# Performance work log

Hardware: AMD Instinct MI355X
Metric: run time of the kernel (lower is better)

The kernel has to match this reference:

```python
import jax, jax.numpy as jnp
import numpy as np
import math

D_MODEL = 256
N_HEAD = 1
C_IN = 32
B, L = 8, 2048
FACTOR = 5


def _pos_encoding(L, D):
    pos = jnp.arange(L, dtype=jnp.float32)[:, None]
    div = jnp.exp(jnp.arange(0, D, 2, dtype=jnp.float32) * (-math.log(10000.0) / D))
    pe = jnp.zeros((L, D), dtype=jnp.float32)
    pe = pe.at[:, 0::2].set(jnp.sin(pos * div))
    pe = pe.at[:, 1::2].set(jnp.cos(pos * div))
    return pe


def _layer_norm(x, g, b, eps=1e-5):
    mu = x.mean(-1, keepdims=True)
    var = ((x - mu) ** 2).mean(-1, keepdims=True)
    return (x - mu) / jnp.sqrt(var + eps) * g + b


def setup_inputs():
    key = jax.random.key(0)
    ks = jax.random.split(key, 16)
    D = D_MODEL
    s = 0.02
    p = {}
    p["x"] = jax.random.normal(ks[0], (B, L, C_IN), jnp.float32)
    sample_k = min(FACTOR * math.ceil(math.log(L)), L)  # = 40 for L=2048
    p["sample_idx"] = jax.random.randint(ks[1], (L, sample_k), 0, L)
    p["emb_w"] = jax.random.normal(ks[2], (C_IN, N_HEAD * D)) * s
    p["emb_b"] = jnp.zeros((N_HEAD * D,))
    for i, n in enumerate(["wq", "wk", "wv", "wo"]):
        p[n] = jax.random.normal(ks[3 + i], (D, D)) * s
        p["b" + n[1]] = jnp.zeros((D,))
    p["conv1_w"] = jax.random.normal(ks[7], (D, D)) * s  # Conv1d kernel=1 == linear, d_ff = d_model
    p["conv1_b"] = jnp.zeros((D,))
    p["conv2_w"] = jax.random.normal(ks[8], (D, D)) * s
    p["conv2_b"] = jnp.zeros((D,))
    for n in ["ln1", "ln2", "lnf"]:
        p[n + "_g"] = jnp.ones((D,))
        p[n + "_b"] = jnp.zeros((D,))
    p["gru_wih"] = jax.random.normal(ks[9], (3 * D, D)) * s
    p["gru_whh"] = jax.random.normal(ks[10], (3 * D, D)) * s
    p["gru_bih"] = jnp.zeros((3 * D,))
    p["gru_bhh"] = jnp.zeros((3 * D,))
    p["fc_w"] = jax.random.normal(ks[11], (D, 1)) * s
    p["fc_b"] = jnp.zeros((1,))
    return p


def _forward(x, sample_idx, emb_w, emb_b, wq, bq, wk, bk, wv, bv, wo, bo,
             conv1_w, conv1_b, conv2_w, conv2_b, ln1_g, ln1_b, ln2_g, ln2_b,
             lnf_g, lnf_b, gru_wih, gru_whh, gru_bih, gru_bhh, fc_w, fc_b):
    Bx, Lx, _ = x.shape
    H = N_HEAD
    src = x @ emb_w + emb_b + _pos_encoding(Lx, emb_w.shape[1])  # [B,L,D]
    D = src.shape[-1]
    dk = D // H

    def heads(t, w, b):
        return (t @ w + b).reshape(Bx, Lx, H, dk).transpose(0, 2, 1, 3)  # [B,H,L,dk]

    Q = heads(src, wq, bq)
    K = heads(src, wk, bk)
    V = heads(src, wv, bv)

    # ---- ProbSparse attention (Informer, non-masked) ----
    u = sample_idx.shape[1]                                  # n_top == sample_k here
    K_sample = K[:, :, sample_idx, :]                        # [B,H,L,s,dk]
    QK_s = jnp.einsum("bhld,bhlsd->bhls", Q, K_sample)
    M = QK_s.max(-1) - QK_s.sum(-1) / Lx                     # sparsity measure per query
    _, top = jax.lax.top_k(M, u)                             # [B,H,u]
    Q_red = jnp.take_along_axis(Q, top[..., None], axis=2)   # [B,H,u,dk]
    scores = jnp.einsum("bhud,bhkd->bhuk", Q_red, K) / jnp.sqrt(jnp.float32(dk))
    attn = jax.nn.softmax(scores, axis=-1)
    upd = jnp.einsum("bhuk,bhkd->bhud", attn, V)             # [B,H,u,dk]
    ctx = jnp.broadcast_to(V.mean(axis=2, keepdims=True), Q.shape)  # initial context = mean(V)
    bi = jnp.arange(Bx)[:, None, None]
    hi = jnp.arange(H)[None, :, None]
    ctx = ctx.at[bi, hi, top].set(upd)
    out = ctx.transpose(0, 2, 1, 3).reshape(Bx, Lx, D) @ wo + bo

    # ---- EncoderLayer FFN (Conv1d k=1 -> gelu -> Conv1d k=1), residuals, norms ----
    x1 = _layer_norm(src + out, ln1_g, ln1_b)
    y = jax.nn.gelu(x1 @ conv1_w + conv1_b, approximate=False)
    y = y @ conv2_w + conv2_b
    enc = _layer_norm(_layer_norm(x1 + y, ln2_g, ln2_b), lnf_g, lnf_b)

    # ---- GRU: faithful to source bug: seq-major nn.GRU fed [B,L,D] -> scans over batch dim ----
    def step(h, xt):
        gi = xt @ gru_wih.T + gru_bih
        gh = h @ gru_whh.T + gru_bhh
        ir, iz, inn = jnp.split(gi, 3, axis=-1)
        hr, hz, hn = jnp.split(gh, 3, axis=-1)
        r = jax.nn.sigmoid(ir + hr)
        z = jax.nn.sigmoid(iz + hz)
        n = jnp.tanh(inn + r * hn)
        h = (1.0 - z) * n + z * h
        return h, h

    h0 = jnp.zeros((Lx, enc.shape[-1]), enc.dtype)
    _, gru_out = jax.lax.scan(step, h0, enc)  # [B,L,D]
    return gru_out[:, -1, :] @ fc_w + fc_b    # [B,1]


def reference(x, sample_idx, emb_w, emb_b, wq, bq, wk, bk, wv, bv, wo, bo,
              conv1_w, conv1_b, conv2_w, conv2_b, ln1_g, ln1_b, ln2_g, ln2_b,
              lnf_g, lnf_b, gru_wih, gru_whh, gru_bih, gru_bhh, fc_w, fc_b):
    return _forward(x, sample_idx, emb_w, emb_b, wq, bq, wk, bk, wv, bv, wo, bo,
                    conv1_w, conv1_b, conv2_w, conv2_b, ln1_g, ln1_b, ln2_g, ln2_b,
                    lnf_g, lnf_b, gru_wih, gru_whh, gru_bih, gru_bhh, fc_w, fc_b)
```

## Files before the change

### kernel.cpp

```cpp
#include <hip/hip_runtime.h>
#include <hip/hip_bf16.h>
#include <math.h>

#define BB 8
#define LL 2048
#define CIN 32
#define DD 256
#define UU 40
#define NROW (BB*LL)
#define NSL  (NROW*DD)
#define GB 8

typedef unsigned short u16;
typedef __attribute__((ext_vector_type(8))) short short8;
typedef __attribute__((ext_vector_type(4))) float f32x4;

__device__ __forceinline__ u16 f2bf(float v) {
    unsigned u = __float_as_uint(v);
    unsigned r = (u + 0x7FFF + ((u >> 16) & 1)) >> 16;
    return (u16)r;
}
__device__ __forceinline__ float bf2f(u16 h) {
    return __uint_as_float(((unsigned)h) << 16);
}

template<int CTRL>
__device__ __forceinline__ float dpp_add(float v) {
    int s = __builtin_amdgcn_update_dpp(0, __float_as_int(v), CTRL, 0xf, 0xf, true);
    return v + __int_as_float(s);
}
__device__ __forceinline__ float row16_sum(float v) {
    v = dpp_add<0x118>(v);
    v = dpp_add<0x114>(v);
    v = dpp_add<0x112>(v);
    v = dpp_add<0x111>(v);
    return v;
}
__device__ __forceinline__ float dot4(float4 a, float4 b) {
    return a.x * b.x + a.y * b.y + a.z * b.z + a.w * b.w;
}
__device__ __forceinline__ float4 nt_load4(const float* p) {
    f32x4 v = __builtin_nontemporal_load((const f32x4*)p);
    float4 r; r.x = v.x; r.y = v.y; r.z = v.z; r.w = v.w;
    return r;
}

__global__ __launch_bounds__(256) void src_kernel(
    const float* __restrict__ x, const float* __restrict__ emb_w,
    const float* __restrict__ emb_b,
    u16* __restrict__ srch, u16* __restrict__ srcl, float* __restrict__ srcrow)
{
    __shared__ float xs[CIN];
    const int orig = blockIdx.x;
    const int b = orig & 7;
    const int l = orig >> 3;
    const int r = (b << 11) | l;
    const int d = threadIdx.x;
    if (d < CIN) xs[d] = x[(size_t)r * CIN + d];
    __syncthreads();
    float acc = emb_b[d];
#pragma unroll 8
    for (int c = 0; c < CIN; ++c) acc += xs[c] * emb_w[c * DD + d];
    const int i = d >> 1;
    const float ang = (float)l * expf((float)(2 * i) * (-9.210340371976184f / 256.0f));
    const float pe = (d & 1) ? cosf(ang) : sinf(ang);
    const float v = acc + pe;
    const u16 h = f2bf(v);
    srch[(size_t)r * DD + d] = h;
    srcl[(size_t)r * DD + d] = f2bf(v - bf2f(h));
    if (l == LL - 1) srcrow[b * DD + d] = v;
}

__global__ __launch_bounds__(256) void splitw_kernel(
    const float* __restrict__ wq, const float* __restrict__ wk,
    const float* __restrict__ wv, u16* __restrict__ whT, u16* __restrict__ wlT)
{
    const int o = blockIdx.x, n = blockIdx.y, k = threadIdx.x;
    const float* W = (o == 0) ? wq : (o == 1) ? wk : wv;
    const float v = W[(size_t)k * DD + n];
    const u16 h = f2bf(v);
    whT[((size_t)o << 16) + n * DD + k] = h;
    wlT[((size_t)o << 16) + n * DD + k] = f2bf(v - bf2f(h));
}

__global__ __launch_bounds__(256) void gemm_qkv_mfma(
    const u16* __restrict__ srch, const u16* __restrict__ srcl,
    const u16* __restrict__ whT, const u16* __restrict__ wlT,
    const float* __restrict__ bq, const float* __restrict__ bk,
    const float* __restrict__ bv,
    float* __restrict__ Qf, float* __restrict__ K, float* __restrict__ V,
    float* __restrict__ qrow)
{
    __shared__ __align__(16) u16 AhS[64][40], AlS[64][40], BhS[64][40], BlS[64][40];
    const int t = threadIdx.x;
    const int bx = blockIdx.x;
    const int mt = (bx & 7) * 32 + (bx >> 3);
    const int bm = mt * 64;
    const int bn = blockIdx.y * 64;
    const int o  = blockIdx.z;
    const u16* wh = whT + ((size_t)o << 16);
    const u16* wl = wlT + ((size_t)o << 16);
    const float* bias = (o == 0) ? bq : (o == 1) ? bk : bv;
    float* C = (o == 0) ? Qf : (o == 1) ? K : V;

    const int srow = t >> 2, sk8 = (t & 3) * 8;
    const int lane = t & 63, w = t >> 6;
    const int frow = lane & 15, kg = (lane >> 4) * 8;

    f32x4 acc[4];
#pragma unroll
    for (int nf = 0; nf < 4; ++nf) acc[nf] = (f32x4){0.f, 0.f, 0.f, 0.f};

    for (int ks = 0; ks < 8; ++ks) {
        const int kb = ks * 32 + sk8;
        *(short8*)&AhS[srow][sk8] = *(const short8*)&srch[(size_t)(bm + srow) * DD + kb];
        *(short8*)&AlS[srow][sk8] = *(const short8*)&srcl[(size_t)(bm + srow) * DD + kb];
        *(short8*)&BhS[srow][sk8] = *(const short8*)&wh[(size_t)(bn + srow) * DD + kb];
        *(short8*)&BlS[srow][sk8] = *(const short8*)&wl[(size_t)(bn + srow) * DD + kb];
        __syncthreads();
        const short8 ah = *(const short8*)&AhS[w * 16 + frow][kg];
        const short8 al = *(const short8*)&AlS[w * 16 + frow][kg];
#pragma unroll
        for (int nf = 0; nf < 4; ++nf) {
            const short8 bh = *(const short8*)&BhS[nf * 16 + frow][kg];
            const short8 bl = *(const short8*)&BlS[nf * 16 + frow][kg];
            acc[nf] = __builtin_amdgcn_mfma_f32_16x16x32_bf16(al, bh, acc[nf], 0, 0, 0);
            acc[nf] = __builtin_amdgcn_mfma_f32_16x16x32_bf16(ah, bl, acc[nf], 0, 0, 0);
            acc[nf] = __builtin_amdgcn_mfma_f32_16x16x32_bf16(ah, bh, acc[nf], 0, 0, 0);
        }
        __syncthreads();
    }
#pragma unroll
    for (int nf = 0; nf < 4; ++nf) {
#pragma unroll
        for (int r = 0; r < 4; ++r) {
            const int row = bm + w * 16 + (lane >> 4) * 4 + r;
            const int col = bn + nf * 16 + (lane & 15);
            const float v = acc[nf][r] + bias[col];
            C[(size_t)row * DD + col] = v;
            if (o == 0 && (row & (LL - 1)) == (LL - 1))
                qrow[(row >> 11) * DD + col] = v;
        }
    }
}

__global__ __launch_bounds__(256, 4) void qks_probe(
    const float* __restrict__ Qf, const float* __restrict__ Kf,
    const int* __restrict__ sidx, float* __restrict__ M)
{
    __shared__ float qk[4][UU];
    const int bid = blockIdx.x;
    const int b = bid & 7;
    const int grp = bid >> 3;
    const int t = threadIdx.x;
    const int wv = t >> 6;
    const int lane = t & 63;
    const int sub = lane >> 4;
    const int j = lane & 15;
    const int l = grp * 4 + wv;
    const size_t r = ((size_t)b << 11) + l;

    const int* si = sidx + (size_t)l * UU;
    const int myidx = __builtin_nontemporal_load(si + (lane < UU ? lane : 0));

    const float* q = &Qf[r * DD];
    const float4 q0 = nt_load4(q + j * 16 + 0);
    const float4 q1 = nt_load4(q + j * 16 + 4);
    const float4 q2 = nt_load4(q + j * 16 + 8);
    const float4 q3 = nt_load4(q + j * 16 + 12);
    const float* Kb = Kf + ((size_t)b << 11) * DD;

    int idxs[UU / 4];
#pragma unroll
    for (int i = 0; i < UU / 4; ++i) idxs[i] = __shfl(myidx, i * 4 + sub);

    float4 kv[5][4];
#pragma unroll
    for (int i = 0; i < 5; ++i) {
        const float4* kr = (const float4*)&Kb[(size_t)idxs[i] * DD] + j * 4;
        kv[i][0] = kr[0]; kv[i][1] = kr[1]; kv[i][2] = kr[2]; kv[i][3] = kr[3];
    }

#pragma unroll
    for (int i = 0; i < UU / 4; ++i) {
        const int s = i % 5;
        float d = dot4(q0, kv[s][0]) + dot4(q1, kv[s][1])
                + dot4(q2, kv[s][2]) + dot4(q3, kv[s][3]);
        if (i + 5 < UU / 4) {
            const float4* kr = (const float4*)&Kb[(size_t)idxs[i + 5] * DD] + j * 4;
            kv[s][0] = kr[0]; kv[s][1] = kr[1]; kv[s][2] = kr[2]; kv[s][3] = kr[3];
        }
        d = row16_sum(d);
        if (j == 15) qk[wv][i * 4 + sub] = d;
    }
    __syncthreads();
    if (t < 4) {
        float mx = -1e30f, sm = 0.0f;
#pragma unroll
        for (int s = 0; s < UU; ++s) { float v = qk[t][s]; mx = fmaxf(mx, v); sm += v; }
        M[((size_t)b << 11) + grp * 4 + t] = mx - sm * (1.0f / (float)LL);
    }
}

__global__ __launch_bounds__(256) void rank_kernel(
    const float* __restrict__ M, int* __restrict__ flag)
{
    __shared__ int redi[256];
    const int b = blockIdx.x, t = threadIdx.x;
    const float* Mb = M + (size_t)b * LL;
    const float ref = Mb[LL - 1];
    int cnt = 0;
    for (int l = t; l < LL; l += 256)
        if (l != LL - 1 && Mb[l] >= ref) cnt++;
    redi[t] = cnt; __syncthreads();
    for (int s = 128; s; s >>= 1) { if (t < s) redi[t] += redi[t + s]; __syncthreads(); }
    if (t == 0) flag[b] = (redi[0] < UU) ? 1 : 0;
}

__global__ __launch_bounds__(256) void ctx_scores(
    const float* __restrict__ qrow, const float* __restrict__ K,
    const int* __restrict__ flag, float* __restrict__ sc)
{
    const int b = blockIdx.x;
    if (!flag[b]) return;
    const int t = threadIdx.x, grp = t >> 4, j = t & 15;
    const size_t base = (size_t)b * LL * DD;
    const float4* qr = (const float4*)&qrow[b * DD];
    const float4 q0 = qr[j * 4 + 0], q1 = qr[j * 4 + 1],
                 q2 = qr[j * 4 + 2], q3 = qr[j * 4 + 3];
    const int k0 = blockIdx.y * 128 + grp * 8;
#pragma unroll
    for (int i = 0; i < 8; ++i) {
        const int k = k0 + i;
        const float4* kr = (const float4*)&K[base + (size_t)k * DD];
        float d = dot4(q0, kr[j * 4 + 0]) + dot4(q1, kr[j * 4 + 1])
                + dot4(q2, kr[j * 4 + 2]) + dot4(q3, kr[j * 4 + 3]);
        d = row16_sum(d);
        if (j == 15) sc[b * LL + k] = d * (1.0f / 16.0f);
    }
}

__global__ __launch_bounds__(256) void ctx_softmax(
    const int* __restrict__ flag, float* __restrict__ sc, float* __restrict__ ssum)
{
    __shared__ float red[256];
    const int b = blockIdx.x;
    if (!flag[b]) return;
    const int t = threadIdx.x;
    float* s = sc + b * LL;
    float lm = -1e30f;
    for (int k = t; k < LL; k += 256) lm = fmaxf(lm, s[k]);
    red[t] = lm; __syncthreads();
    for (int st = 128; st; st >>= 1) { if (t < st) red[t] = fmaxf(red[t], red[t + st]); __syncthreads(); }
    const float mx = red[0]; __syncthreads();
    float ls = 0.0f;
    for (int k = t; k < LL; k += 256) { float e = expf(s[k] - mx); s[k] = e; ls += e; }
    red[t] = ls; __syncthreads();
    for (int st = 128; st; st >>= 1) { if (t < st) red[t] += red[t + st]; __syncthreads(); }
    if (t == 0) ssum[b] = red[0];
}

__global__ __launch_bounds__(256) void ctx_pv(
    const float* __restrict__ V, const float* __restrict__ sc,
    const int* __restrict__ flag, float* __restrict__ part)
{
    const int b = blockIdx.x, slice = blockIdx.y;
    const int d = threadIdx.x;
    const size_t base = (size_t)b * LL * DD;
    const int k0 = slice * 256;
    float acc = 0.0f;
    if (flag[b]) {
#pragma unroll 4
        for (int k = k0; k < k0 + 256; ++k)
            acc += sc[b * LL + k] * V[base + (size_t)k * DD + d];
    } else {
#pragma unroll 4
        for (int k = k0; k < k0 + 256; ++k)
            acc += V[base + (size_t)k * DD + d];
    }
    part[(b * 8 + slice) * DD + d] = acc;
}

__device__ __forceinline__ float block_sum256(float v, float* red) {
    const int t = threadIdx.x;
    __syncthreads();
    red[t] = v; __syncthreads();
    for (int s = 128; s; s >>= 1) { if (t < s) red[t] += red[t + s]; __syncthreads(); }
    return red[0];
}

__global__ __launch_bounds__(256) void tail_kernel(
    const float* __restrict__ srcrow, const float* __restrict__ part,
    const float* __restrict__ ssum, const int* __restrict__ flag,
    const float* __restrict__ wo, const float* __restrict__ bo,
    const float* __restrict__ c1w, const float* __restrict__ c1b,
    const float* __restrict__ c2w, const float* __restrict__ c2b,
    const float* __restrict__ g1, const float* __restrict__ b1,
    const float* __restrict__ g2, const float* __restrict__ b2,
    const float* __restrict__ gf, const float* __restrict__ bf,
    float* __restrict__ enc)
{
    __shared__ float xs[DD];
    __shared__ float red[DD];
    const int b = blockIdx.x, d = threadIdx.x;

    float cv = 0.0f;
#pragma unroll
    for (int i = 0; i < 8; ++i) cv += part[(b * 8 + i) * DD + d];
    cv = flag[b] ? cv / ssum[b] : cv * (1.0f / (float)LL);

    xs[d] = cv; __syncthreads();
    float o = bo[d];
    for (int j = 0; j < DD; ++j) o += xs[j] * wo[j * DD + d];
    const float v = srcrow[b * DD + d] + o;

    float mu = block_sum256(v, red) * (1.0f / DD);
    float dv = v - mu;
    float var = block_sum256(dv * dv, red) * (1.0f / DD);
    const float x1 = dv * rsqrtf(var + 1e-5f) * g1[d] + b1[d];

    __syncthreads(); xs[d] = x1; __syncthreads();
    float a = c1b[d];
    for (int j = 0; j < DD; ++j) a += xs[j] * c1w[j * DD + d];
    a = 0.5f * a * (1.0f + erff(a * 0.70710678118654752f));

    __syncthreads(); xs[d] = a; __syncthreads();
    float y = c2b[d];
    for (int j = 0; j < DD; ++j) y += xs[j] * c2w[j * DD + d];

    float t2 = x1 + y;
    mu = block_sum256(t2, red) * (1.0f / DD);
    dv = t2 - mu;
    var = block_sum256(dv * dv, red) * (1.0f / DD);
    float t3 = dv * rsqrtf(var + 1e-5f) * g2[d] + b2[d];

    mu = block_sum256(t3, red) * (1.0f / DD);
    dv = t3 - mu;
    var = block_sum256(dv * dv, red) * (1.0f / DD);
    enc[b * DD + d] = dv * rsqrtf(var + 1e-5f) * gf[d] + bf[d];
}

__global__ __launch_bounds__(768) void gru_coop_kernel(
    const float* __restrict__ enc, const float* __restrict__ wih,
    const float* __restrict__ whh, const float* __restrict__ bih,
    const float* __restrict__ bhh, const float* __restrict__ fcw,
    const float* __restrict__ fcb,
    unsigned long long* __restrict__ hpub,
    float* __restrict__ out)
{
    __shared__ float whhS[96][257];
    __shared__ float encS[BB][260];
    __shared__ float giS[96][8];
    __shared__ float hS[DD];
    __shared__ float ghS[96];
    __shared__ float red[256];
    const int g = blockIdx.x, t = threadIdx.x;

#pragma unroll
    for (int i = 0; i < 8; ++i) {
        const int f4 = t + 768 * i;
        const int lr = f4 >> 6, c4 = f4 & 63;
        const int R = (lr >> 5) * 256 + g * 32 + (lr & 31);
        const float4 w = *(const float4*)&whh[(size_t)R * DD + c4 * 4];
        whhS[lr][c4 * 4 + 0] = w.x; whhS[lr][c4 * 4 + 1] = w.y;
        whhS[lr][c4 * 4 + 2] = w.z; whhS[lr][c4 * 4 + 3] = w.w;
    }
    for (int e = t; e < BB * DD; e += 768) encS[e >> 8][e & 255] = enc[e];
    if (t < DD) hS[t] = 0.0f;
    __syncthreads();

    {
        const int lr = t >> 3, b = t & 7;
        const int R = (lr >> 5) * 256 + g * 32 + (lr & 31);
        float acc = bih[R];
        const float4* w4 = (const float4*)&wih[(size_t)R * DD];
#pragma unroll 8
        for (int jc = 0; jc < 64; ++jc) {
            const float4 w = w4[jc];
            acc += encS[b][jc * 4 + 0] * w.x + encS[b][jc * 4 + 1] * w.y
                 + encS[b][jc * 4 + 2] * w.z + encS[b][jc * 4 + 3] * w.w;
        }
        giS[lr][b] = acc;
    }
    __syncthreads();

    for (int step = 1; step <= BB; ++step) {
        const int b = step - 1;
        const int lr = t >> 3, s = t & 7;
        float p = 0.0f;
#pragma unroll
        for (int k = 0; k < 32; ++k) {
            const int c = s * 32 + ((k + s * 4) & 31);
            p += whhS[lr][c] * hS[c];
        }
        p = dpp_add<0x114>(p); p = dpp_add<0x112>(p); p = dpp_add<0x111>(p);
        if (s == 7) ghS[lr] = p + bhh[(lr >> 5) * 256 + g * 32 + (lr & 31)];
        __syncthreads();

        if (t < 32) {
            const float r  = 1.0f / (1.0f + expf(-(giS[t][b]      + ghS[t])));
            const float z  = 1.0f / (1.0f + expf(-(giS[32 + t][b] + ghS[32 + t])));
            const float n  = tanhf(giS[64 + t][b] + r * ghS[64 + t]);
            const float hnew = (1.0f - z) * n + z * hS[g * 32 + t];
            const unsigned long long w =
                ((unsigned long long)(unsigned)step << 32) | (unsigned long long)__float_as_uint(hnew);
            __hip_atomic_store(&hpub[g * 32 + t], w, __ATOMIC_RELAXED, __HIP_MEMORY_SCOPE_AGENT);
        }
        __syncthreads();
        if (t < DD) {
            unsigned long long w;
            do {
                w = __hip_atomic_load(&hpub[t], __ATOMIC_RELAXED, __HIP_MEMORY_SCOPE_AGENT);
            } while ((int)(w >> 32) != step);
            hS[t] = __uint_as_float((unsigned)w);
        }
        __syncthreads();

        if (g == 0) {
            if (t < DD) red[t] = hS[t] * fcw[t];
            __syncthreads();
            for (int st2 = 128; st2; st2 >>= 1) { if (t < st2) red[t] += red[t + st2]; __syncthreads(); }
            if (t == 0) out[b] = red[0] + fcb[0];
            __syncthreads();
        }
    }
}

extern "C" void kernel_launch(void* const* d_in, const int* in_sizes, int n_in,
                              void* d_out, int out_size, void* d_ws, size_t ws_size,
                              hipStream_t stream)
{
    const float* x      = (const float*)d_in[0];
    const int*   sidx   = (const int*)  d_in[1];
    const float* emb_w  = (const float*)d_in[2];
    const float* emb_b  = (const float*)d_in[3];
    const float* wq     = (const float*)d_in[4];
    const float* bq     = (const float*)d_in[5];
    const float* wk     = (const float*)d_in[6];
    const float* bk     = (const float*)d_in[7];
    const float* wv     = (const float*)d_in[8];
    const float* bv     = (const float*)d_in[9];
    const float* wo     = (const float*)d_in[10];
    const float* bo     = (const float*)d_in[11];
    const float* c1w    = (const float*)d_in[12];
    const float* c1b    = (const float*)d_in[13];
    const float* c2w    = (const float*)d_in[14];
    const float* c2b    = (const float*)d_in[15];
    const float* ln1g   = (const float*)d_in[16];
    const float* ln1b   = (const float*)d_in[17];
    const float* ln2g   = (const float*)d_in[18];
    const float* ln2b   = (const float*)d_in[19];
    const float* lnfg   = (const float*)d_in[20];
    const float* lnfb   = (const float*)d_in[21];
    const float* wih    = (const float*)d_in[22];
    const float* whh    = (const float*)d_in[23];
    const float* bih    = (const float*)d_in[24];
    const float* bhh    = (const float*)d_in[25];
    const float* fcw    = (const float*)d_in[26];
    const float* fcb    = (const float*)d_in[27];

    float* ws  = (float*)d_ws;
    float* K    = ws;
    float* V    = K + NSL;
    float* Mv   = V + NSL;
    int*   flag = (int*)(Mv + NROW);
    float* sc   = (float*)(flag + 16);
    float* ssum = sc + BB * LL;
    float* part = ssum + 16;
    float* srcrow = part + BB * 8 * DD;
    float* qrow = srcrow + BB * DD;
    float* enc  = qrow + BB * DD;
    unsigned long long* hpub = (unsigned long long*)(enc + BB * DD);
    u16* srch = (u16*)(hpub + 256);
    u16* srcl = srch + NSL;
    u16* whT  = srcl + NSL;
    u16* wlT  = whT + 3 * 65536;
    float* Qf = (float*)(wlT + 3 * 65536);

    hipMemsetAsync(hpub, 0, 256 * sizeof(unsigned long long), stream);

    splitw_kernel<<<dim3(3, 256), 256, 0, stream>>>(wq, wk, wv, whT, wlT);
    src_kernel<<<NROW, 256, 0, stream>>>(x, emb_w, emb_b, srch, srcl, srcrow);
    gemm_qkv_mfma<<<dim3(256, 4, 3), 256, 0, stream>>>(srch, srcl, whT, wlT,
                                                       bq, bk, bv, Qf, K, V, qrow);
    qks_probe<<<NROW / 4, 256, 0, stream>>>(Qf, K, sidx, Mv);
    rank_kernel<<<BB, 256, 0, stream>>>(Mv, flag);
    ctx_scores<<<dim3(BB, 16), 256, 0, stream>>>(qrow, K, flag, sc);
    ctx_softmax<<<BB, 256, 0, stream>>>(flag, sc, ssum);
    ctx_pv<<<dim3(BB, 8), 256, 0, stream>>>(V, sc, flag, part);
    tail_kernel<<<BB, 256, 0, stream>>>(srcrow, part, ssum, flag, wo, bo,
                                        c1w, c1b, c2w, c2b,
                                        ln1g, ln1b, ln2g, ln2b, lnfg, lnfb, enc);
    gru_coop_kernel<<<GB, 768, 0, stream>>>(enc, wih, whh, bih, bhh, fcw, fcb,
                                            hpub, (float*)d_out);
}
```

Measured before the change: 195.7 us.

## Stage sampled K rows into LDS via async global_load_lds in probe kernel

The Q·K sample probe now runs one 64-thread block per query row instead of four wavefronts per block. All 40 sampled K rows are issued up front as direct global-to-LDS loads. Computation is staggered with explicit vmcnt waits, so each group of four rows is consumed as it arrives, which raises memory-level parallelism compared with the register-held five-deep prefetch. In exchange it uses 40 KB of LDS per single-wave block, which limits how many blocks fit per CU, and it quadruples the block count.

```diff
diff --git a/kernel.cpp b/kernel.cpp
--- a/kernel.cpp
+++ b/kernel.cpp
@@ -43,6 +43,15 @@
     f32x4 v = __builtin_nontemporal_load((const f32x4*)p);
     float4 r; r.x = v.x; r.y = v.y; r.z = v.z; r.w = v.w;
     return r;
+}
+__device__ __forceinline__ void gload_lds16(const float* g, float* l) {
+    __builtin_amdgcn_global_load_lds(
+        (const __attribute__((address_space(1))) float*)g,
+        (__attribute__((address_space(3))) float*)l, 16, 0, 0);
+}
+template<int N> __device__ __forceinline__ void wait_vmcnt() {
+    asm volatile("s_waitcnt vmcnt(%0)" :: "n"(N) : "memory");
+    __builtin_amdgcn_sched_barrier(0);
 }
 
 __global__ __launch_bounds__(256) void src_kernel(
@@ -144,61 +153,64 @@
     }
 }
 
-__global__ __launch_bounds__(256, 4) void qks_probe(
+__global__ __launch_bounds__(64) void qks_probe(
     const float* __restrict__ Qf, const float* __restrict__ Kf,
     const int* __restrict__ sidx, float* __restrict__ M)
 {
-    __shared__ float qk[4][UU];
+    __shared__ __align__(16) float Ks[UU][256];
+    __shared__ float qk[UU];
     const int bid = blockIdx.x;
     const int b = bid & 7;
-    const int grp = bid >> 3;
+    const int l = bid >> 3;
     const int t = threadIdx.x;
-    const int wv = t >> 6;
-    const int lane = t & 63;
-    const int sub = lane >> 4;
-    const int j = lane & 15;
-    const int l = grp * 4 + wv;
-    const size_t r = ((size_t)b << 11) + l;
+    const int sub = t >> 4, j = t & 15;
 
     const int* si = sidx + (size_t)l * UU;
-    const int myidx = __builtin_nontemporal_load(si + (lane < UU ? lane : 0));
-
-    const float* q = &Qf[r * DD];
+    const int myidx = si[t < UU ? t : 0];
+
+    const float* q = &Qf[(((size_t)b << 11) + l) * DD];
     const float4 q0 = nt_load4(q + j * 16 + 0);
     const float4 q1 = nt_load4(q + j * 16 + 4);
     const float4 q2 = nt_load4(q + j * 16 + 8);
     const float4 q3 = nt_load4(q + j * 16 + 12);
+
     const float* Kb = Kf + ((size_t)b << 11) * DD;
-
-    int idxs[UU / 4];
-#pragma unroll
-    for (int i = 0; i < UU / 4; ++i) idxs[i] = __shfl(myidx, i * 4 + sub);
-
-    float4 kv[5][4];
-#pragma unroll
-    for (int i = 0; i < 5; ++i) {
-        const float4* kr = (const float4*)&Kb[(size_t)idxs[i] * DD] + j * 4;
-        kv[i][0] = kr[0]; kv[i][1] = kr[1]; kv[i][2] = kr[2]; kv[i][3] = kr[3];
-    }
-
-#pragma unroll
-    for (int i = 0; i < UU / 4; ++i) {
-        const int s = i % 5;
-        float d = dot4(q0, kv[s][0]) + dot4(q1, kv[s][1])
-                + dot4(q2, kv[s][2]) + dot4(q3, kv[s][3]);
-        if (i + 5 < UU / 4) {
-            const float4* kr = (const float4*)&Kb[(size_t)idxs[i + 5] * DD] + j * 4;
-            kv[s][0] = kr[0]; kv[s][1] = kr[1]; kv[s][2] = kr[2]; kv[s][3] = kr[3];
-        }
+    const int coff = 16 * j + 4 * sub;
+
+#pragma unroll
+    for (int s = 0; s < UU; ++s) {
+        const int idx = __builtin_amdgcn_readlane(myidx, s);
+        gload_lds16(Kb + (size_t)idx * DD + coff, &Ks[s][0]);
+    }
+
+    auto cg = [&](int i) {
+        const int sm = i * 4 + sub;
+        const float4 kv0 = *(const float4*)&Ks[sm][0 * 64 + j * 4];
+        const float4 kv1 = *(const float4*)&Ks[sm][1 * 64 + j * 4];
+        const float4 kv2 = *(const float4*)&Ks[sm][2 * 64 + j * 4];
+        const float4 kv3 = *(const float4*)&Ks[sm][3 * 64 + j * 4];
+        float d = dot4(q0, kv0) + dot4(q1, kv1)
+                + dot4(q2, kv2) + dot4(q3, kv3);
         d = row16_sum(d);
-        if (j == 15) qk[wv][i * 4 + sub] = d;
-    }
+        if (j == 15) qk[sm] = d;
+    };
+    wait_vmcnt<36>(); cg(0);
+    wait_vmcnt<32>(); cg(1);
+    wait_vmcnt<28>(); cg(2);
+    wait_vmcnt<24>(); cg(3);
+    wait_vmcnt<20>(); cg(4);
+    wait_vmcnt<16>(); cg(5);
+    wait_vmcnt<12>(); cg(6);
+    wait_vmcnt<8>();  cg(7);
+    wait_vmcnt<4>();  cg(8);
+    wait_vmcnt<0>();  cg(9);
+
     __syncthreads();
-    if (t < 4) {
+    if (t == 0) {
         float mx = -1e30f, sm = 0.0f;
 #pragma unroll
-        for (int s = 0; s < UU; ++s) { float v = qk[t][s]; mx = fmaxf(mx, v); sm += v; }
-        M[((size_t)b << 11) + grp * 4 + t] = mx - sm * (1.0f / (float)LL);
+        for (int s = 0; s < UU; ++s) { float v = qk[s]; mx = fmaxf(mx, v); sm += v; }
+        M[((size_t)b << 11) + l] = mx - sm * (1.0f / (float)LL);
     }
 }
 
@@ -483,7 +495,7 @@
     src_kernel<<<NROW, 256, 0, stream>>>(x, emb_w, emb_b, srch, srcl, srcrow);
     gemm_qkv_mfma<<<dim3(256, 4, 3), 256, 0, stream>>>(srch, srcl, whT, wlT,
                                                        bq, bk, bv, Qf, K, V, qrow);
-    qks_probe<<<NROW / 4, 256, 0, stream>>>(Qf, K, sidx, Mv);
+    qks_probe<<<NROW, 64, 0, stream>>>(Qf, K, sidx, Mv);
     rank_kernel<<<BB, 256, 0, stream>>>(Mv, flag);
     ctx_scores<<<dim3(BB, 16), 256, 0, stream>>>(qrow, K, flag, sc);
     ctx_softmax<<<BB, 256, 0, stream>>>(flag, sc, ssum);
```

Result: slower. 216.1 us (+10.4%).

## Compute sparsity probe with bf16 keys plus error bounds and exact recheck

Applied to the files above, without the earlier changes.

The QK sampling probe now reads a bf16 copy of K, which the QKV GEMM writes out, and computes an error bound for each row from absolute-value dot products. A classify pass counts rows that are certainly at or above the last row's exact measure and collects uncertain rows, which a recheck kernel then recomputes in fp32. This halves the gather bandwidth of the probe, at the cost of extra bf16 K writes, two more launches and atomics. Correctness depends on the 0.0025 error bound covering bf16 rounding of K and on the uncertain list fitting within the cap.

```diff
diff --git a/kernel.cpp b/kernel.cpp
--- a/kernel.cpp
+++ b/kernel.cpp
@@ -10,6 +10,7 @@
 #define NROW (BB*LL)
 #define NSL  (NROW*DD)
 #define GB 8
+#define UNCAP 1024
 
 typedef unsigned short u16;
 typedef __attribute__((ext_vector_type(8))) short short8;
@@ -43,6 +44,29 @@
     f32x4 v = __builtin_nontemporal_load((const f32x4*)p);
     float4 r; r.x = v.x; r.y = v.y; r.z = v.z; r.w = v.w;
     return r;
+}
+
+__device__ __forceinline__ void exact_row_qk(
+    const float* __restrict__ q, const float* __restrict__ Kb,
+    const int* __restrict__ si, int lane, int sub, int j,
+    float* qkrow)
+{
+    const int myidx = si[lane < UU ? lane : 0];
+    const float4 q0 = nt_load4(q + j * 16 + 0);
+    const float4 q1 = nt_load4(q + j * 16 + 4);
+    const float4 q2 = nt_load4(q + j * 16 + 8);
+    const float4 q3 = nt_load4(q + j * 16 + 12);
+    int idxs[UU / 4];
+#pragma unroll
+    for (int i = 0; i < UU / 4; ++i) idxs[i] = __shfl(myidx, i * 4 + sub);
+#pragma unroll
+    for (int i = 0; i < UU / 4; ++i) {
+        const float4* kr = (const float4*)&Kb[(size_t)idxs[i] * DD];
+        float d = dot4(q0, kr[j * 4 + 0]) + dot4(q1, kr[j * 4 + 1])
+                + dot4(q2, kr[j * 4 + 2]) + dot4(q3, kr[j * 4 + 3]);
+        d = row16_sum(d);
+        if (j == 15) qkrow[i * 4 + sub] = d;
+    }
 }
 
 __global__ __launch_bounds__(256) void src_kernel(
@@ -89,7 +113,7 @@
     const float* __restrict__ bq, const float* __restrict__ bk,
     const float* __restrict__ bv,
     float* __restrict__ Qf, float* __restrict__ K, float* __restrict__ V,
-    float* __restrict__ qrow)
+    float* __restrict__ qrow, u16* __restrict__ Khb)
 {
     __shared__ __align__(16) u16 AhS[64][40], AlS[64][40], BhS[64][40], BlS[64][40];
     const int t = threadIdx.x;
@@ -140,89 +164,154 @@
             C[(size_t)row * DD + col] = v;
             if (o == 0 && (row & (LL - 1)) == (LL - 1))
                 qrow[(row >> 11) * DD + col] = v;
-        }
-    }
-}
-
-__global__ __launch_bounds__(256, 4) void qks_probe(
-    const float* __restrict__ Qf, const float* __restrict__ Kf,
-    const int* __restrict__ sidx, float* __restrict__ M)
+            if (o == 1)
+                Khb[(size_t)row * DD + col] = f2bf(v);
+        }
+    }
+}
+
+__global__ __launch_bounds__(256) void qks_pass1(
+    const float* __restrict__ Qf, const u16* __restrict__ Khb,
+    const float* __restrict__ Kf, const int* __restrict__ sidx,
+    float* __restrict__ Mt, float* __restrict__ Eb,
+    float* __restrict__ M2047ex)
 {
     __shared__ float qk[4][UU];
+    __shared__ float qas[4][UU];
+    const int t = threadIdx.x;
+    const int wv = t >> 6, lane = t & 63, sub = lane >> 4, j = lane & 15;
     const int bid = blockIdx.x;
+
+    if (bid >= NROW / 4) {
+        const int b = (bid - NROW / 4) * 4 + wv;
+        const int l = LL - 1;
+        exact_row_qk(&Qf[(((size_t)b << 11) + l) * DD],
+                     Kf + ((size_t)b << 11) * DD,
+                     sidx + (size_t)l * UU, lane, sub, j, qk[wv]);
+        __syncthreads();
+        if (t < 4) {
+            const int bb = (bid - NROW / 4) * 4 + t;
+            float mx = -1e30f, sm = 0.0f;
+#pragma unroll
+            for (int s = 0; s < UU; ++s) { float v = qk[t][s]; mx = fmaxf(mx, v); sm += v; }
+            M2047ex[bb] = mx - sm * (1.0f / (float)LL);
+        }
+        return;
+    }
+
     const int b = bid & 7;
     const int grp = bid >> 3;
-    const int t = threadIdx.x;
-    const int wv = t >> 6;
-    const int lane = t & 63;
-    const int sub = lane >> 4;
-    const int j = lane & 15;
     const int l = grp * 4 + wv;
     const size_t r = ((size_t)b << 11) + l;
-
     const int* si = sidx + (size_t)l * UU;
     const int myidx = __builtin_nontemporal_load(si + (lane < UU ? lane : 0));
 
     const float* q = &Qf[r * DD];
-    const float4 q0 = nt_load4(q + j * 16 + 0);
-    const float4 q1 = nt_load4(q + j * 16 + 4);
-    const float4 q2 = nt_load4(q + j * 16 + 8);
-    const float4 q3 = nt_load4(q + j * 16 + 12);
-    const float* Kb = Kf + ((size_t)b << 11) * DD;
+    const float4 qa0 = nt_load4(q + j * 8);
+    const float4 qa1 = nt_load4(q + j * 8 + 4);
+    const float4 qb0 = nt_load4(q + 128 + j * 8);
+    const float4 qb1 = nt_load4(q + 128 + j * 8 + 4);
+    float qA[8] = {qa0.x, qa0.y, qa0.z, qa0.w, qa1.x, qa1.y, qa1.z, qa1.w};
+    float qB[8] = {qb0.x, qb0.y, qb0.z, qb0.w, qb1.x, qb1.y, qb1.z, qb1.w};
+    const u16* Khbb = Khb + (((size_t)b << 11)) * DD;
 
     int idxs[UU / 4];
 #pragma unroll
     for (int i = 0; i < UU / 4; ++i) idxs[i] = __shfl(myidx, i * 4 + sub);
 
-    float4 kv[5][4];
-#pragma unroll
-    for (int i = 0; i < 5; ++i) {
-        const float4* kr = (const float4*)&Kb[(size_t)idxs[i] * DD] + j * 4;
-        kv[i][0] = kr[0]; kv[i][1] = kr[1]; kv[i][2] = kr[2]; kv[i][3] = kr[3];
-    }
-
 #pragma unroll
     for (int i = 0; i < UU / 4; ++i) {
-        const int s = i % 5;
-        float d = dot4(q0, kv[s][0]) + dot4(q1, kv[s][1])
-                + dot4(q2, kv[s][2]) + dot4(q3, kv[s][3]);
-        if (i + 5 < UU / 4) {
-            const float4* kr = (const float4*)&Kb[(size_t)idxs[i + 5] * DD] + j * 4;
-            kv[s][0] = kr[0]; kv[s][1] = kr[1]; kv[s][2] = kr[2]; kv[s][3] = kr[3];
-        }
-        d = row16_sum(d);
-        if (j == 15) qk[wv][i * 4 + sub] = d;
+        const u16* kr = &Khbb[(size_t)idxs[i] * DD];
+        const short8 k0 = *(const short8*)(kr + j * 8);
+        const short8 k1 = *(const short8*)(kr + 128 + j * 8);
+        float d = 0.0f, da = 0.0f;
+#pragma unroll
+        for (int m = 0; m < 8; ++m) {
+            const float k0v = bf2f((u16)k0[m]);
+            const float k1v = bf2f((u16)k1[m]);
+            d  = fmaf(qA[m], k0v, d);
+            da = fmaf(fabsf(qA[m]), fabsf(k0v), da);
+            d  = fmaf(qB[m], k1v, d);
+            da = fmaf(fabsf(qB[m]), fabsf(k1v), da);
+        }
+        d  = row16_sum(d);
+        da = row16_sum(da);
+        if (j == 15) { qk[wv][i * 4 + sub] = d; qas[wv][i * 4 + sub] = da; }
     }
     __syncthreads();
     if (t < 4) {
-        float mx = -1e30f, sm = 0.0f;
-#pragma unroll
-        for (int s = 0; s < UU; ++s) { float v = qk[t][s]; mx = fmaxf(mx, v); sm += v; }
-        M[((size_t)b << 11) + grp * 4 + t] = mx - sm * (1.0f / (float)LL);
-    }
-}
-
-__global__ __launch_bounds__(256) void rank_kernel(
-    const float* __restrict__ M, int* __restrict__ flag)
+        float mx = -1e30f, sm = 0.0f, ma = 0.0f;
+#pragma unroll
+        for (int s = 0; s < UU; ++s) {
+            float v = qk[t][s]; mx = fmaxf(mx, v); sm += v;
+            ma = fmaxf(ma, qas[t][s]);
+        }
+        const size_t rr = ((size_t)b << 11) + grp * 4 + t;
+        Mt[rr] = mx - sm * (1.0f / (float)LL);
+        Eb[rr] = ma * 0.0025f;
+    }
+}
+
+__global__ __launch_bounds__(256) void classify_kernel(
+    const float* __restrict__ Mt, const float* __restrict__ Eb,
+    const float* __restrict__ M2047ex,
+    int* __restrict__ ge_cnt, int* __restrict__ unc_cnt, int* __restrict__ unc_list)
 {
     __shared__ int redi[256];
     const int b = blockIdx.x, t = threadIdx.x;
-    const float* Mb = M + (size_t)b * LL;
-    const float ref = Mb[LL - 1];
-    int cnt = 0;
-    for (int l = t; l < LL; l += 256)
-        if (l != LL - 1 && Mb[l] >= ref) cnt++;
-    redi[t] = cnt; __syncthreads();
+    const float Mx = M2047ex[b];
+    int cge = 0;
+    for (int l = t; l < LL; l += 256) {
+        if (l == LL - 1) continue;
+        const size_t r = ((size_t)b << 11) + l;
+        const float m = Mt[r], e = Eb[r];
+        if (m - e >= Mx) cge++;
+        else if (m + e >= Mx) {
+            const int slot = atomicAdd(&unc_cnt[b], 1);
+            if (slot < UNCAP) unc_list[b * UNCAP + slot] = l;
+        }
+    }
+    redi[t] = cge; __syncthreads();
     for (int s = 128; s; s >>= 1) { if (t < s) redi[t] += redi[t + s]; __syncthreads(); }
-    if (t == 0) flag[b] = (redi[0] < UU) ? 1 : 0;
+    if (t == 0) ge_cnt[b] = redi[0];
+}
+
+__global__ __launch_bounds__(256) void recheck_kernel(
+    const float* __restrict__ Qf, const float* __restrict__ Kf,
+    const int* __restrict__ sidx, const float* __restrict__ M2047ex,
+    const int* __restrict__ unc_cnt, const int* __restrict__ unc_list,
+    int* __restrict__ ge_cnt)
+{
+    __shared__ float qk[4][UU];
+    const int b = blockIdx.y;
+    int cnt = unc_cnt[b]; cnt = cnt < UNCAP ? cnt : UNCAP;
+    if ((int)blockIdx.x * 4 >= cnt) return;
+    const int t = threadIdx.x;
+    const int wv = t >> 6, lane = t & 63, sub = lane >> 4, j = lane & 15;
+    const int slot = blockIdx.x * 4 + wv;
+    const int l = (slot < cnt) ? unc_list[b * UNCAP + slot] : 0;
+    exact_row_qk(&Qf[(((size_t)b << 11) + l) * DD],
+                 Kf + ((size_t)b << 11) * DD,
+                 sidx + (size_t)l * UU, lane, sub, j, qk[wv]);
+    __syncthreads();
+    if (t < 4) {
+        const int slot2 = blockIdx.x * 4 + t;
+        if (slot2 < cnt) {
+            float mx = -1e30f, sm = 0.0f;
+#pragma unroll
+            for (int s = 0; s < UU; ++s) { float v = qk[t][s]; mx = fmaxf(mx, v); sm += v; }
+            const float Ml = mx - sm * (1.0f / (float)LL);
+            if (Ml >= M2047ex[b]) atomicAdd(&ge_cnt[b], 1);
+        }
+    }
 }
 
 __global__ __launch_bounds__(256) void ctx_scores(
     const float* __restrict__ qrow, const float* __restrict__ K,
-    const int* __restrict__ flag, float* __restrict__ sc)
+    const int* __restrict__ ge_cnt, float* __restrict__ sc)
 {
     const int b = blockIdx.x;
-    if (!flag[b]) return;
+    if (ge_cnt[b] >= UU) return;
     const int t = threadIdx.x, grp = t >> 4, j = t & 15;
     const size_t base = (size_t)b * LL * DD;
     const float4* qr = (const float4*)&qrow[b * DD];
@@ -241,11 +330,11 @@
 }
 
 __global__ __launch_bounds__(256) void ctx_softmax(
-    const int* __restrict__ flag, float* __restrict__ sc, float* __restrict__ ssum)
+    const int* __restrict__ ge_cnt, float* __restrict__ sc, float* __restrict__ ssum)
 {
     __shared__ float red[256];
     const int b = blockIdx.x;
-    if (!flag[b]) return;
+    if (ge_cnt[b] >= UU) return;
     const int t = threadIdx.x;
     float* s = sc + b * LL;
     float lm = -1e30f;
@@ -262,14 +351,14 @@
 
 __global__ __launch_bounds__(256) void ctx_pv(
     const float* __restrict__ V, const float* __restrict__ sc,
-    const int* __restrict__ flag, float* __restrict__ part)
+    const int* __restrict__ ge_cnt, float* __restrict__ part)
 {
     const int b = blockIdx.x, slice = blockIdx.y;
     const int d = threadIdx.x;
     const size_t base = (size_t)b * LL * DD;
     const int k0 = slice * 256;
     float acc = 0.0f;
-    if (flag[b]) {
+    if (ge_cnt[b] < UU) {
 #pragma unroll 4
         for (int k = k0; k < k0 + 256; ++k)
             acc += sc[b * LL + k] * V[base + (size_t)k * DD + d];
@@ -291,7 +380,7 @@
 
 __global__ __launch_bounds__(256) void tail_kernel(
     const float* __restrict__ srcrow, const float* __restrict__ part,
-    const float* __restrict__ ssum, const int* __restrict__ flag,
+    const float* __restrict__ ssum, const int* __restrict__ ge_cnt,
     const float* __restrict__ wo, const float* __restrict__ bo,
     const float* __restrict__ c1w, const float* __restrict__ c1b,
     const float* __restrict__ c2w, const float* __restrict__ c2b,
@@ -307,7 +396,7 @@
     float cv = 0.0f;
 #pragma unroll
     for (int i = 0; i < 8; ++i) cv += part[(b * 8 + i) * DD + d];
-    cv = flag[b] ? cv / ssum[b] : cv * (1.0f / (float)LL);
+    cv = (ge_cnt[b] < UU) ? cv / ssum[b] : cv * (1.0f / (float)LL);
 
     xs[d] = cv; __syncthreads();
     float o = bo[d];
@@ -463,32 +552,44 @@
     float* K    = ws;
     float* V    = K + NSL;
     float* Mv   = V + NSL;
-    int*   flag = (int*)(Mv + NROW);
-    float* sc   = (float*)(flag + 16);
+    float* Eb   = Mv + NROW;
+    float* sc   = Eb + NROW;
     float* ssum = sc + BB * LL;
     float* part = ssum + 16;
     float* srcrow = part + BB * 8 * DD;
     float* qrow = srcrow + BB * DD;
     float* enc  = qrow + BB * DD;
-    unsigned long long* hpub = (unsigned long long*)(enc + BB * DD);
-    u16* srch = (u16*)(hpub + 256);
+    float* M2047ex = enc + BB * DD;
+    int*   ge_cnt  = (int*)(M2047ex + 16);
+    int*   unc_list = ge_cnt + 8;
+    unsigned long long* hpub = (unsigned long long*)(unc_list + BB * UNCAP);
+    int*   unc_cnt = (int*)(hpub + 256);
+    u16* srch = (u16*)(unc_cnt + 8);
     u16* srcl = srch + NSL;
     u16* whT  = srcl + NSL;
     u16* wlT  = whT + 3 * 65536;
     float* Qf = (float*)(wlT + 3 * 65536);
-
-    hipMemsetAsync(hpub, 0, 256 * sizeof(unsigned long long), stream);
+    u16* Khb  = (u16*)(Qf + NSL);
+
+    hipMemsetAsync(hpub, 0, 256 * sizeof(unsigned long long) + 8 * sizeof(int),
+                   stream);
 
     splitw_kernel<<<dim3(3, 256), 256, 0, stream>>>(wq, wk, wv, whT, wlT);
     src_kernel<<<NROW, 256, 0, stream>>>(x, emb_w, emb_b, srch, srcl, srcrow);
     gemm_qkv_mfma<<<dim3(256, 4, 3), 256, 0, stream>>>(srch, srcl, whT, wlT,
-                                                       bq, bk, bv, Qf, K, V, qrow);
-    qks_probe<<<NROW / 4, 256, 0, stream>>>(Qf, K, sidx, Mv);
-    rank_kernel<<<BB, 256, 0, stream>>>(Mv, flag);
-    ctx_scores<<<dim3(BB, 16), 256, 0, stream>>>(qrow, K, flag, sc);
-    ctx_softmax<<<BB, 256, 0, stream>>>(flag, sc, ssum);
-    ctx_pv<<<dim3(BB, 8), 256, 0, stream>>>(V, sc, flag, part);
-    tail_kernel<<<BB, 256, 0, stream>>>(srcrow, part, ssum, flag, wo, bo,
+                                                       bq, bk, bv, Qf, K, V,
+                                                       qrow, Khb);
+    qks_pass1<<<NROW / 4 + 2, 256, 0, stream>>>(Qf, Khb, K, sidx, Mv, Eb,
+                                                M2047ex);
+    classify_kernel<<<BB, 256, 0, stream>>>(Mv, Eb, M2047ex, ge_cnt, unc_cnt,
+                                            unc_list);
+    recheck_kernel<<<dim3(UNCAP / 4, BB), 256, 0, stream>>>(Qf, K, sidx,
+                                                            M2047ex, unc_cnt,
+                                                            unc_list, ge_cnt);
+    ctx_scores<<<dim3(BB, 16), 256, 0, stream>>>(qrow, K, ge_cnt, sc);
+    ctx_softmax<<<BB, 256, 0, stream>>>(ge_cnt, sc, ssum);
+    ctx_pv<<<dim3(BB, 8), 256, 0, stream>>>(V, sc, ge_cnt, part);
+    tail_kernel<<<BB, 256, 0, stream>>>(srcrow, part, ssum, ge_cnt, wo, bo,
                                         c1w, c1b, c2w, c2b,
                                         ln1g, ln1b, ln2g, ln2b, lnfg, lnfb, enc);
     gru_coop_kernel<<<GB, 768, 0, stream>>>(enc, wih, whh, bih, bhh, fcw, fcb,
```

Result: slower. 200.9 us (+2.7%).
